# Optimization experiments

Hardware: AMD Instinct MI355X
Metric: run time of the kernel (lower is better)

Reference implementation:

```python
import jax, jax.numpy as jnp
import numpy as np

B, D, N, H = 4, 256, 2048, 4
HEAD_DIM = D // H


def conv1x1(W, b, x):
    # Conv1d(kernel_size=1): [B, Cin, N] -> [B, Cout, N]
    return jnp.einsum('oi,bin->bon', W, x) + b[None, :, None]


def setup_inputs() -> dict:
    key = jax.random.key(0)
    ks = jax.random.split(key, 8)
    s = 0.05
    return {
        'x': jax.random.normal(ks[0], (B, D, N), jnp.float32),
        'source': jax.random.normal(ks[1], (B, D, N), jnp.float32),
        'edge': jax.random.uniform(ks[2], (B, N, N), jnp.float32),
        'Wq': jax.random.normal(ks[3], (D, D), jnp.float32) * s,
        'bq': jnp.zeros((D,), jnp.float32),
        'Wk': jax.random.normal(ks[4], (D, D), jnp.float32) * s,
        'bk': jnp.zeros((D,), jnp.float32),
        'Wv': jax.random.normal(ks[5], (D, D), jnp.float32) * s,
        'bv': jnp.zeros((D,), jnp.float32),
        'Wm': jax.random.normal(ks[6], (D, D), jnp.float32) * s,
        'bm': jnp.zeros((D,), jnp.float32),
        'W1': jax.random.normal(ks[7], (2 * D, 2 * D), jnp.float32) * s,
        'b1': jnp.zeros((2 * D,), jnp.float32),
        'W2': jax.random.normal(jax.random.fold_in(key, 99), (D, 2 * D), jnp.float32) * s,
        'b2': jnp.zeros((D,), jnp.float32),
    }


def reference(x, source, edge, Wq, bq, Wk, bk, Wv, bv, Wm, bm, W1, b1, W2, b2):
    b = x.shape[0]
    # projections, then split channels D -> (head_dim, H), matching torch .view
    q = conv1x1(Wq, bq, x).reshape(b, HEAD_DIM, H, -1)       # [B, d, H, N]
    k = conv1x1(Wk, bk, source).reshape(b, HEAD_DIM, H, -1)  # [B, d, H, M]
    v = conv1x1(Wv, bv, source).reshape(b, HEAD_DIM, H, -1)
    scores = jnp.einsum('bdhn,bdhm->bhnm', q, k) / jnp.sqrt(jnp.float32(HEAD_DIM))
    prob = jax.nn.softmax(scores, axis=-1) * edge[:, None, :, :]  # edge-weighted probs
    msg = jnp.einsum('bhnm,bdhm->bdhn', prob, v).reshape(b, D, -1)
    message = conv1x1(Wm, bm, msg)                           # merge heads
    h = jnp.concatenate([x, message], axis=1)                # [B, 2D, N]
    h = jax.nn.relu(conv1x1(W1, b1, h))
    return conv1x1(W2, b2, h)                                # [B, D, N]
```

## Files before the change

kernel.cpp:

```cpp
#include <hip/hip_runtime.h>
#include <math.h>

#define B_ 4
#define D_ 256
#define N_ 2048
#define H_ 4

typedef __attribute__((ext_vector_type(8))) __bf16 bf16x8;
typedef __attribute__((ext_vector_type(4))) __bf16 bf16x4;
typedef __attribute__((ext_vector_type(4))) float f32x4;

__device__ __forceinline__ void load_row16(const float* src, bf16x8* xs) {
    float tmp[16];
    *(float4*)&tmp[0]  = *(const float4*)&src[0];
    *(float4*)&tmp[4]  = *(const float4*)&src[4];
    *(float4*)&tmp[8]  = *(const float4*)&src[8];
    *(float4*)&tmp[12] = *(const float4*)&src[12];
    __bf16* o = (__bf16*)xs;
#pragma unroll
    for (int i = 0; i < 16; ++i) o[i] = (__bf16)tmp[i];
}
__device__ __forceinline__ void load_row16(const __bf16* src, bf16x8* xs) {
    xs[0] = *(const bf16x8*)src;
    xs[1] = *(const bf16x8*)(src + 8);
}

template <typename In1T, typename In2T, typename OutT>
__device__ __forceinline__ void conv_tile(
    const In1T* __restrict__ in1, int C1,
    const In2T* __restrict__ in2, int C2,
    const float* __restrict__ Wt, const float* __restrict__ bias,
    OutT* __restrict__ out, int Cout, int K, int RELU, float oscale,
    int b, int o0, int n0, __bf16 (*sXT)[72])
{
    const int t = threadIdx.x;
    const int w  = t >> 6;
    const int g  = (t >> 4) & 3;
    const int c16 = t & 15;
    const int d_ld = t & 63;
    const int xcol = (t >> 6) * 16;

    f32x4 acc[4];
#pragma unroll
    for (int i = 0; i < 4; ++i) acc[i] = (f32x4){0.f, 0.f, 0.f, 0.f};

    bf16x8 xs[2];
    float4 wreg[4];
    const int ow = o0 + 16 * w + c16;

    auto LOADX = [&](int ks) {
        const int ch = ks + d_ld;
        if (ch < C1) load_row16(in1 + ((size_t)b * C1 + ch) * N_ + n0 + xcol, xs);
        else         load_row16(in2 + ((size_t)b * C2 + (ch - C1)) * N_ + n0 + xcol, xs);
    };
    auto LOADW = [&](int ks) {
        wreg[0] = *(const float4*)&Wt[(size_t)ow * K + ks + 8 * g];
        wreg[1] = *(const float4*)&Wt[(size_t)ow * K + ks + 8 * g + 4];
        wreg[2] = *(const float4*)&Wt[(size_t)ow * K + ks + 32 + 8 * g];
        wreg[3] = *(const float4*)&Wt[(size_t)ow * K + ks + 32 + 8 * g + 4];
    };
    auto WRITEXT = [&](int buf) {
        __bf16 (*sx)[72] = sXT + (size_t)buf * 64;
        const __bf16* kp = (const __bf16*)xs;
#pragma unroll
        for (int i = 0; i < 16; ++i)
            sx[xcol + i][d_ld] = kp[i];
    };

    LOADX(0);
    LOADW(0);
    WRITEXT(0);
    __syncthreads();

    const int nsteps = K >> 6;
    for (int s = 0; s < nsteps; ++s) {
        const int cur = s & 1;
        const int ks = s << 6;
        if (s + 1 < nsteps) LOADX(ks + 64);

        bf16x8 af[2];
#pragma unroll
        for (int kc = 0; kc < 2; ++kc) {
            const float* w0 = (const float*)&wreg[2 * kc];
            const float* w1 = (const float*)&wreg[2 * kc + 1];
#pragma unroll
            for (int i = 0; i < 4; ++i) {
                af[kc][i]     = (__bf16)w0[i];
                af[kc][i + 4] = (__bf16)w1[i];
            }
        }
        if (s + 1 < nsteps) LOADW(ks + 64);

        __bf16 (*sx)[72] = sXT + (size_t)cur * 64;
#pragma unroll
        for (int kc = 0; kc < 2; ++kc)
#pragma unroll
            for (int nsub = 0; nsub < 4; ++nsub) {
                const bf16x8 bfr = *(const bf16x8*)&sx[16 * nsub + c16][32 * kc + 8 * g];
                acc[nsub] = __builtin_amdgcn_mfma_f32_16x16x32_bf16(af[kc], bfr, acc[nsub], 0, 0, 0);
            }

        if (s + 1 < nsteps) WRITEXT(cur ^ 1);
        __syncthreads();
    }

#pragma unroll
    for (int nsub = 0; nsub < 4; ++nsub)
#pragma unroll
        for (int r = 0; r < 4; ++r) {
            const int o = o0 + 16 * w + 4 * g + r;
            float v = acc[nsub][r] + bias[o];
            if (RELU) v = fmaxf(v, 0.f);
            v *= oscale;
            out[((size_t)b * Cout + o) * N_ + n0 + 16 * nsub + c16] = (OutT)v;
        }
}

__global__ __launch_bounds__(256) void conv_hh_kernel(
    const __bf16* __restrict__ in1, const float* __restrict__ W,
    const float* __restrict__ bias, __bf16* __restrict__ out, int Cout, int K)
{
    __shared__ __bf16 sXT[2 * 64][72];
    conv_tile<__bf16, __bf16, __bf16>(in1, K, (const __bf16*)nullptr, 0,
        W, bias, out, Cout, K, 0, 1.0f,
        blockIdx.z, blockIdx.y * 64, blockIdx.x * 64, sXT);
}

__global__ __launch_bounds__(256) void conv_mix_kernel(
    const float* __restrict__ in1, int C1,
    const __bf16* __restrict__ in2, int C2,
    const float* __restrict__ W, const float* __restrict__ bias,
    __bf16* __restrict__ out, int Cout, int K)
{
    __shared__ __bf16 sXT[2 * 64][72];
    conv_tile<float, __bf16, __bf16>(in1, C1, in2, C2,
        W, bias, out, Cout, K, 1, 1.0f,
        blockIdx.z, blockIdx.y * 64, blockIdx.x * 64, sXT);
}

__global__ __launch_bounds__(256) void conv_hf_kernel(
    const __bf16* __restrict__ in1, const float* __restrict__ W,
    const float* __restrict__ bias, float* __restrict__ out, int Cout, int K)
{
    __shared__ __bf16 sXT[2 * 64][72];
    conv_tile<__bf16, __bf16, float>(in1, K, (const __bf16*)nullptr, 0,
        W, bias, out, Cout, K, 0, 1.0f,
        blockIdx.z, blockIdx.y * 64, blockIdx.x * 64, sXT);
}

__global__ __launch_bounds__(256) void qkv_conv_kernel(
    const float* __restrict__ x, const float* __restrict__ source,
    const float* __restrict__ Wq, const float* __restrict__ bq,
    const float* __restrict__ Wk, const float* __restrict__ bk,
    const float* __restrict__ Wv, const float* __restrict__ bv,
    __bf16* __restrict__ Qo, __bf16* __restrict__ Ko, __bf16* __restrict__ Vo)
{
    __shared__ __bf16 sXT[2 * 64][72];
    const int sel = blockIdx.y >> 2;
    const int o0  = (blockIdx.y & 3) * 64;
    const float* in = (sel == 0) ? x : source;
    const float* W  = (sel == 0) ? Wq : (sel == 1) ? Wk : Wv;
    const float* bs = (sel == 0) ? bq : (sel == 1) ? bk : bv;
    __bf16* out     = (sel == 0) ? Qo : (sel == 1) ? Ko : Vo;
    const float sc  = (sel == 1) ? 0.125f * 1.4426950408889634f : 1.0f;
    conv_tile<float, float, __bf16>(in, D_, (const float*)nullptr, 0,
        W, bs, out, D_, D_, 0, sc,
        blockIdx.z, o0, blockIdx.x * 64, sXT);
}

template <int NSPLIT>
__global__ __launch_bounds__(256, 4) void attn_kernel(
    const __bf16* __restrict__ Qg, const __bf16* __restrict__ Kg,
    const __bf16* __restrict__ Vg, const float* __restrict__ Eg,
    __bf16* __restrict__ OP, float* __restrict__ ML)
{
    const int nt    = blockIdx.x;
    const int n0    = nt * 64;
    const int split = blockIdx.y % NSPLIT;
    const int h     = blockIdx.y / NSPLIT;
    const int b     = blockIdx.z;
    const int t  = threadIdx.x;
    const int w  = t >> 6;
    const int g  = (t >> 4) & 3;
    const int c16 = t & 15;

    const int MT   = 32 / NSPLIT;
    const int m_lo = split * (N_ / NSPLIT);
    const int pid  = ((b * H_ + h) * NSPLIT + split) * 32 + nt;

    __shared__ __bf16 sKT[2][64][72];
    __shared__ __bf16 sP [2][64][72];

    bf16x8 qf[2];
#pragma unroll
    for (int kc = 0; kc < 2; ++kc)
#pragma unroll
        for (int e = 0; e < 8; ++e) {
            const int d = 32 * kc + 8 * g + e;
            qf[kc][e] = Qg[((size_t)b * D_ + d * H_ + h) * N_ + n0 + 16 * w + c16];
        }

    f32x4 acc[4];
#pragma unroll
    for (int i = 0; i < 4; ++i) acc[i] = (f32x4){0.f, 0.f, 0.f, 0.f};
    float Lr[4];
#pragma unroll
    for (int r = 0; r < 4; ++r) Lr[r] = 0.f;

    const int kd = t >> 2;
    const int km = (t & 3) * 16;
    const size_t kbase = ((size_t)b * D_ + kd * H_ + h) * N_ + m_lo + km;
    const size_t vrow  = ((size_t)b * D_ + (16 * w + c16) * H_ + h) * N_ + m_lo;
    const size_t ebase = ((size_t)b * N_ + n0 + 16 * w + 4 * g) * N_ + m_lo + c16;

    bf16x8 kreg[2];
    bf16x8 vreg[2];
    float  ereg[4][4];

    auto LOADK = [&](int m0) {
        kreg[0] = *(const bf16x8*)&Kg[kbase + m0];
        kreg[1] = *(const bf16x8*)&Kg[kbase + m0 + 8];
    };
    auto LOADV = [&](int m0) {
        vreg[0] = *(const bf16x8*)&Vg[vrow + m0 + 8 * g];
        vreg[1] = *(const bf16x8*)&Vg[vrow + m0 + 32 + 8 * g];
    };
    auto LOADE = [&](int m0) {
#pragma unroll
        for (int r = 0; r < 4; ++r)
#pragma unroll
            for (int ms = 0; ms < 4; ++ms)
                ereg[r][ms] = Eg[ebase + (size_t)r * N_ + m0 + 16 * ms];
    };
    const int kcb = kd >> 3, kcw = kd & 7;
    auto WRITEKT = [&](int buf) {
        const __bf16* kp = (const __bf16*)kreg;
#pragma unroll
        for (int i = 0; i < 16; ++i) {
            const int m = km + i;
            sKT[buf][m][(((kcb ^ ((m >> 3) & 7)) << 3) | kcw)] = kp[i];
        }
    };

    LOADK(0);
    LOADV(0);
    LOADE(0);
    WRITEKT(0);
    __syncthreads();

    for (int mt = 0; mt < MT; ++mt) {
        const int cur = mt & 1;
        const int m0n = (mt < MT - 1 ? mt + 1 : mt) * 64;

        const bf16x8 af0 = vreg[0], af1 = vreg[1];
        LOADK(m0n);
        LOADV(m0n);

        f32x4 sfrag[4];
#pragma unroll
        for (int msub = 0; msub < 4; ++msub) {
            const int m   = 16 * msub + c16;
            const int swz = (m >> 3) & 7;
            f32x4 s = (f32x4){0.f, 0.f, 0.f, 0.f};
#pragma unroll
            for (int kc = 0; kc < 2; ++kc) {
                const bf16x8 bfr = *(const bf16x8*)&sKT[cur][m][((4 * kc + g) ^ swz) << 3];
                s = __builtin_amdgcn_mfma_f32_16x16x32_bf16(qf[kc], bfr, s, 0, 0, 0);
            }
            sfrag[msub] = s;
        }

        {
            const int pc_hi = c16 >> 3, pc_lo = c16 & 7;
#pragma unroll
            for (int msub = 0; msub < 4; ++msub) {
#pragma unroll
                for (int r = 0; r < 4; ++r) {
                    const int nloc = 16 * w + 4 * g + r;
                    const int swz  = (nloc >> 3) & 7;
                    const float p = exp2f(sfrag[msub][r]);
                    Lr[r] += p;
                    sP[cur][nloc][((((2 * msub + pc_hi) ^ swz) << 3) | pc_lo)] =
                        (__bf16)(p * ereg[r][msub]);
                }
            }
        }
        LOADE(m0n);

        WRITEKT(cur ^ 1);
        __syncthreads();

#pragma unroll
        for (int nsub = 0; nsub < 4; ++nsub) {
            const int row = 16 * nsub + c16;
            const int swz = (row >> 3) & 7;
            const bf16x8 b0 = *(const bf16x8*)&sP[cur][row][(g ^ swz) << 3];
            acc[nsub] = __builtin_amdgcn_mfma_f32_16x16x32_bf16(af0, b0, acc[nsub], 0, 0, 0);
            const bf16x8 b1 = *(const bf16x8*)&sP[cur][row][((4 + g) ^ swz) << 3];
            acc[nsub] = __builtin_amdgcn_mfma_f32_16x16x32_bf16(af1, b1, acc[nsub], 0, 0, 0);
        }
    }

#pragma unroll
    for (int mask = 1; mask < 16; mask <<= 1)
#pragma unroll
        for (int r = 0; r < 4; ++r) Lr[r] += __shfl_xor(Lr[r], mask);
    if (c16 == 0) {
#pragma unroll
        for (int r = 0; r < 4; ++r) {
            const int nloc = 16 * w + 4 * g + r;
            ML[(size_t)pid * 128 + nloc]      = 0.0f;
            ML[(size_t)pid * 128 + 64 + nloc] = Lr[r];
        }
    }
#pragma unroll
    for (int nsub = 0; nsub < 4; ++nsub)
#pragma unroll
        for (int r = 0; r < 4; ++r) {
            const int dd = 16 * w + 4 * g + r;
            OP[(size_t)pid * 4096 + dd * 64 + 16 * nsub + c16] = (__bf16)acc[nsub][r];
        }
}

template <int NSPLIT>
__global__ __launch_bounds__(256) void combine_kernel(
    const __bf16* __restrict__ OP, const float* __restrict__ ML,
    __bf16* __restrict__ msg)
{
    const int nt = blockIdx.x;
    const int h  = blockIdx.y;
    const int b  = blockIdx.z;
    const int t  = threadIdx.x;
    const int d  = t & 63;
    const int seg = t >> 6;
    const int pid0 = ((b * H_ + h) * NSPLIT) * 32 + nt;

    __shared__ float sM[NSPLIT][64], sL[NSPLIT][64];
    if (t < NSPLIT * 64) {
        const int s = t >> 6, n = t & 63;
        sM[s][n] = ML[(size_t)(pid0 + s * 32) * 128 + n];
        sL[s][n] = ML[(size_t)(pid0 + s * 32) * 128 + 64 + n];
    }
    __syncthreads();

#pragma unroll
    for (int q = 0; q < 4; ++q) {
        const int c0 = seg * 16 + q * 4;
        float o[4] = {0.f, 0.f, 0.f, 0.f};
        float wgt[NSPLIT][4];
#pragma unroll
        for (int j = 0; j < 4; ++j) {
            float mx = -3.0e38f;
            for (int s = 0; s < NSPLIT; ++s) mx = fmaxf(mx, sM[s][c0 + j]);
            float den = 0.f;
            for (int s = 0; s < NSPLIT; ++s) {
                wgt[s][j] = __expf(sM[s][c0 + j] - mx);
                den += wgt[s][j] * sL[s][c0 + j];
            }
            const float inv = 1.0f / den;
            for (int s = 0; s < NSPLIT; ++s) wgt[s][j] *= inv;
        }
        for (int s = 0; s < NSPLIT; ++s) {
            const bf16x4 a = *(const bf16x4*)&OP[(size_t)(pid0 + s * 32) * 4096 + d * 64 + c0];
#pragma unroll
            for (int j = 0; j < 4; ++j) o[j] += wgt[s][j] * (float)a[j];
        }
        bf16x4 r;
#pragma unroll
        for (int j = 0; j < 4; ++j) r[j] = (__bf16)o[j];
        *(bf16x4*)&msg[((size_t)b * D_ + d * H_ + h) * N_ + nt * 64 + c0] = r;
    }
}

extern "C" void kernel_launch(void* const* d_in, const int* in_sizes, int n_in,
                              void* d_out, int out_size, void* d_ws, size_t ws_size,
                              hipStream_t stream) {
    const float* x      = (const float*)d_in[0];
    const float* source = (const float*)d_in[1];
    const float* edge   = (const float*)d_in[2];
    const float* Wq = (const float*)d_in[3];
    const float* bq = (const float*)d_in[4];
    const float* Wk = (const float*)d_in[5];
    const float* bk = (const float*)d_in[6];
    const float* Wv = (const float*)d_in[7];
    const float* bv = (const float*)d_in[8];
    const float* Wm = (const float*)d_in[9];
    const float* bm = (const float*)d_in[10];
    const float* W1 = (const float*)d_in[11];
    const float* b1 = (const float*)d_in[12];
    const float* W2 = (const float*)d_in[13];
    const float* b2 = (const float*)d_in[14];
    float* out = (float*)d_out;

    const size_t BDN = (size_t)B_ * D_ * N_;
    char* p = (char*)d_ws;
    __bf16* Qh  = (__bf16*)(p);
    __bf16* Kh  = (__bf16*)(p + 2 * BDN);
    __bf16* Vh  = (__bf16*)(p + 4 * BDN);
    __bf16* MSG = (__bf16*)(p + 6 * BDN);
    __bf16* MES = (__bf16*)(p + 8 * BDN);
    __bf16* H1  = (__bf16*)(p + 10 * BDN);
    char*   tail = p + 14 * BDN;
    const size_t baseBytes = 14 * BDN;

    const dim3 blk(256);
    const dim3 gD(N_ / 64, D_ / 64, B_);
    const dim3 g2D(N_ / 64, 2 * D_ / 64, B_);

    qkv_conv_kernel<<<dim3(N_ / 64, 12, B_), blk, 0, stream>>>(
        x, source, Wq, bq, Wk, bk, Wv, bv, Qh, Kh, Vh);

    auto needFor = [&](int ns) {
        const size_t pids = (size_t)ns * B_ * H_ * 32;
        return baseBytes + pids * 4096 * 2 + pids * 128 * 4;
    };
    if (ws_size >= needFor(2)) {
        const size_t pids = (size_t)2 * B_ * H_ * 32;
        __bf16* OP = (__bf16*)tail;
        float*  ML = (float*)(tail + pids * 4096 * 2);
        attn_kernel<2><<<dim3(32, H_ * 2, B_), blk, 0, stream>>>(Qh, Kh, Vh, edge, OP, ML);
        combine_kernel<2><<<dim3(32, H_, B_), blk, 0, stream>>>(OP, ML, MSG);
    } else {
        const size_t pids = (size_t)B_ * H_ * 32;
        __bf16* OP = (__bf16*)tail;
        float*  ML = (float*)(tail + pids * 4096 * 2);
        attn_kernel<1><<<dim3(32, H_, B_), blk, 0, stream>>>(Qh, Kh, Vh, edge, OP, ML);
        combine_kernel<1><<<dim3(32, H_, B_), blk, 0, stream>>>(OP, ML, MSG);
    }

    conv_hh_kernel<<<gD, blk, 0, stream>>>(MSG, Wm, bm, MES, D_, D_);
    conv_mix_kernel<<<g2D, blk, 0, stream>>>(x, D_, MES, D_, W1, b1, H1, 2 * D_, 2 * D_);
    conv_hf_kernel<<<gD, blk, 0, stream>>>(H1, W2, b2, out, D_, 2 * D_);
}
```

Baseline: 128.3 us.

## Fold merge-head conv weights into first MLP conv via precomputed W1·Wm

Precomputes a fused weight matrix Wcat = [W1_x | W1_m·Wm] and a fused bias b1 + W1_m·bm in a small per-call kernel. The merge-head conv kernel and its intermediate buffer are removed, and the MLP first layer reads the attention message directly. This removes one full conv pass and one bf16 round trip of the activation tensor, at the cost of a tiny weight GEMM each call and slightly different rounding, since the message is no longer rounded to bf16 after the merge.

```diff
diff --git a/kernel.cpp b/kernel.cpp
--- a/kernel.cpp
+++ b/kernel.cpp
@@ -114,16 +114,6 @@
             v *= oscale;
             out[((size_t)b * Cout + o) * N_ + n0 + 16 * nsub + c16] = (OutT)v;
         }
-}
-
-__global__ __launch_bounds__(256) void conv_hh_kernel(
-    const __bf16* __restrict__ in1, const float* __restrict__ W,
-    const float* __restrict__ bias, __bf16* __restrict__ out, int Cout, int K)
-{
-    __shared__ __bf16 sXT[2 * 64][72];
-    conv_tile<__bf16, __bf16, __bf16>(in1, K, (const __bf16*)nullptr, 0,
-        W, bias, out, Cout, K, 0, 1.0f,
-        blockIdx.z, blockIdx.y * 64, blockIdx.x * 64, sXT);
 }
 
 __global__ __launch_bounds__(256) void conv_mix_kernel(
@@ -166,6 +156,75 @@
     conv_tile<float, float, __bf16>(in, D_, (const float*)nullptr, 0,
         W, bs, out, D_, D_, 0, sc,
         blockIdx.z, o0, blockIdx.x * 64, sXT);
+}
+
+__global__ __launch_bounds__(256) void wfuse_kernel(
+    const float* __restrict__ W1, const float* __restrict__ Wm,
+    const float* __restrict__ bm, const float* __restrict__ b1,
+    float* __restrict__ Wcat, float* __restrict__ bfused)
+{
+    const int t = threadIdx.x;
+    if (blockIdx.y == 8) {
+        if (blockIdx.x < 2) {
+            const int o = blockIdx.x * 256 + t;
+            float a = b1[o];
+            for (int k = 0; k < 256; ++k)
+                a += W1[(size_t)o * 512 + 256 + k] * bm[k];
+            bfused[o] = a;
+        }
+        return;
+    }
+    const int o0 = blockIdx.y * 64;
+    const int c0 = blockIdx.x * 64;
+    const int tr = t >> 4, tc = t & 15;
+    if (c0 < 256) {
+#pragma unroll
+        for (int i = 0; i < 4; ++i) {
+            const int o = o0 + tr * 4 + i;
+            const float4 v = *(const float4*)&W1[(size_t)o * 512 + c0 + tc * 4];
+            *(float4*)&Wcat[(size_t)o * 512 + c0 + tc * 4] = v;
+        }
+        return;
+    }
+    __shared__ float sA[16][68];
+    __shared__ float sW[16][68];
+    float acc[4][4];
+#pragma unroll
+    for (int i = 0; i < 4; ++i)
+#pragma unroll
+        for (int j = 0; j < 4; ++j) acc[i][j] = 0.f;
+    const int wo = t & 63, wk = (t >> 6) * 4;
+    const int kr = t >> 4, cc = t & 15;
+    for (int k0 = 0; k0 < 256; k0 += 16) {
+        __syncthreads();
+        {
+            const float4 a = *(const float4*)&W1[(size_t)(o0 + wo) * 512 + 256 + k0 + wk];
+            sA[wk + 0][wo] = a.x; sA[wk + 1][wo] = a.y;
+            sA[wk + 2][wo] = a.z; sA[wk + 3][wo] = a.w;
+        }
+        {
+            const float4 wv = *(const float4*)&Wm[(size_t)(k0 + kr) * 256 + (c0 - 256) + cc * 4];
+            *(float4*)&sW[kr][cc * 4] = wv;
+        }
+        __syncthreads();
+#pragma unroll
+        for (int k = 0; k < 16; ++k) {
+            const float4 av = *(const float4*)&sA[k][tr * 4];
+            const float4 wv = *(const float4*)&sW[k][tc * 4];
+            const float aa[4] = {av.x, av.y, av.z, av.w};
+            const float ww[4] = {wv.x, wv.y, wv.z, wv.w};
+#pragma unroll
+            for (int i = 0; i < 4; ++i)
+#pragma unroll
+                for (int j = 0; j < 4; ++j)
+                    acc[i][j] = fmaf(aa[i], ww[j], acc[i][j]);
+        }
+    }
+#pragma unroll
+    for (int i = 0; i < 4; ++i) {
+        float4 r = {acc[i][0], acc[i][1], acc[i][2], acc[i][3]};
+        *(float4*)&Wcat[(size_t)(o0 + tr * 4 + i) * 512 + c0 + tc * 4] = r;
+    }
 }
 
 template <int NSPLIT>
@@ -398,37 +457,40 @@
     __bf16* Kh  = (__bf16*)(p + 2 * BDN);
     __bf16* Vh  = (__bf16*)(p + 4 * BDN);
     __bf16* MSG = (__bf16*)(p + 6 * BDN);
-    __bf16* MES = (__bf16*)(p + 8 * BDN);
-    __bf16* H1  = (__bf16*)(p + 10 * BDN);
-    char*   tail = p + 14 * BDN;
-    const size_t baseBytes = 14 * BDN;
+    __bf16* H1  = (__bf16*)(p + 8 * BDN);
+    char*   tail = p + 12 * BDN;
+    const size_t baseBytes = 12 * BDN;
 
     const dim3 blk(256);
     const dim3 gD(N_ / 64, D_ / 64, B_);
     const dim3 g2D(N_ / 64, 2 * D_ / 64, B_);
 
+    auto needFor = [&](int ns) {
+        const size_t pids = (size_t)ns * B_ * H_ * 32;
+        return baseBytes + pids * 4096 * 2 + pids * 128 * 4
+             + (size_t)512 * 512 * 4 + 512 * 4;
+    };
+
+    const int NS = (ws_size >= needFor(2)) ? 2 : 1;
+    const size_t pids = (size_t)NS * B_ * H_ * 32;
+    __bf16* OP = (__bf16*)tail;
+    float*  ML = (float*)(tail + pids * 4096 * 2);
+    float*  Wcat   = (float*)(tail + pids * 4096 * 2 + pids * 128 * 4);
+    float*  bfused = Wcat + (size_t)512 * 512;
+
+    wfuse_kernel<<<dim3(8, 9), blk, 0, stream>>>(W1, Wm, bm, b1, Wcat, bfused);
+
     qkv_conv_kernel<<<dim3(N_ / 64, 12, B_), blk, 0, stream>>>(
         x, source, Wq, bq, Wk, bk, Wv, bv, Qh, Kh, Vh);
 
-    auto needFor = [&](int ns) {
-        const size_t pids = (size_t)ns * B_ * H_ * 32;
-        return baseBytes + pids * 4096 * 2 + pids * 128 * 4;
-    };
-    if (ws_size >= needFor(2)) {
-        const size_t pids = (size_t)2 * B_ * H_ * 32;
-        __bf16* OP = (__bf16*)tail;
-        float*  ML = (float*)(tail + pids * 4096 * 2);
+    if (NS == 2) {
         attn_kernel<2><<<dim3(32, H_ * 2, B_), blk, 0, stream>>>(Qh, Kh, Vh, edge, OP, ML);
         combine_kernel<2><<<dim3(32, H_, B_), blk, 0, stream>>>(OP, ML, MSG);
     } else {
-        const size_t pids = (size_t)B_ * H_ * 32;
-        __bf16* OP = (__bf16*)tail;
-        float*  ML = (float*)(tail + pids * 4096 * 2);
         attn_kernel<1><<<dim3(32, H_, B_), blk, 0, stream>>>(Qh, Kh, Vh, edge, OP, ML);
         combine_kernel<1><<<dim3(32, H_, B_), blk, 0, stream>>>(OP, ML, MSG);
     }
 
-    conv_hh_kernel<<<gD, blk, 0, stream>>>(MSG, Wm, bm, MES, D_, D_);
-    conv_mix_kernel<<<g2D, blk, 0, stream>>>(x, D_, MES, D_, W1, b1, H1, 2 * D_, 2 * D_);
+    conv_mix_kernel<<<g2D, blk, 0, stream>>>(x, D_, MSG, D_, Wcat, bfused, H1, 2 * D_, 2 * D_);
     conv_hf_kernel<<<gD, blk, 0, stream>>>(H1, W2, b2, out, D_, 2 * D_);
 }
```

Result: slower. 137.0 us (+6.7%).

## Fuse split-combine of attention partials into message merge conv

Applied to the files above, without the earlier changes.

Removes the separate combine kernel and folds the combining of the attention split partials into the Wm 1x1 conv's input loader. The loader sums the partial outputs and divides by the summed L, which assumes the partial maxima are zero (attn writes M=0, since the softmax needs no max shift here). This drops one launch and the write/read round trip of the MSG buffer. In exchange, each conv block re-reads the partials and ML, and does that redundantly across the 4 output-channel tile blocks.

```diff
diff --git a/kernel.cpp b/kernel.cpp
--- a/kernel.cpp
+++ b/kernel.cpp
@@ -116,14 +116,132 @@
         }
 }
 
-__global__ __launch_bounds__(256) void conv_hh_kernel(
-    const __bf16* __restrict__ in1, const float* __restrict__ W,
-    const float* __restrict__ bias, __bf16* __restrict__ out, int Cout, int K)
+template <int NS>
+__global__ __launch_bounds__(256) void conv_msg_kernel(
+    const __bf16* __restrict__ OP, const float* __restrict__ ML,
+    const float* __restrict__ Wt, const float* __restrict__ bias,
+    __bf16* __restrict__ out)
 {
     __shared__ __bf16 sXT[2 * 64][72];
-    conv_tile<__bf16, __bf16, __bf16>(in1, K, (const __bf16*)nullptr, 0,
-        W, bias, out, Cout, K, 0, 1.0f,
-        blockIdx.z, blockIdx.y * 64, blockIdx.x * 64, sXT);
+    const int t = threadIdx.x;
+    const int w  = t >> 6;
+    const int g  = (t >> 4) & 3;
+    const int c16 = t & 15;
+    const int d_ld = t & 63;
+    const int xcol = (t >> 6) * 16;
+    const int nt = blockIdx.x;
+    const int n0 = nt * 64;
+    const int o0 = blockIdx.y * 64;
+    const int b  = blockIdx.z;
+    const int K = D_, Cout = D_;
+
+    const int h = d_ld & 3;
+    const size_t pid0 = ((size_t)(b * H_ + h) * NS) * 32 + nt;
+
+    float invL[16];
+#pragma unroll
+    for (int i = 0; i < 16; i += 4) {
+        float4 a = *(const float4*)&ML[pid0 * 128 + 64 + xcol + i];
+        if (NS == 2) {
+            const float4 c = *(const float4*)&ML[(pid0 + 32) * 128 + 64 + xcol + i];
+            a.x += c.x; a.y += c.y; a.z += c.z; a.w += c.w;
+        }
+        invL[i + 0] = 1.0f / a.x; invL[i + 1] = 1.0f / a.y;
+        invL[i + 2] = 1.0f / a.z; invL[i + 3] = 1.0f / a.w;
+    }
+
+    f32x4 acc[4];
+#pragma unroll
+    for (int i = 0; i < 4; ++i) acc[i] = (f32x4){0.f, 0.f, 0.f, 0.f};
+
+    bf16x8 xs[2];
+    float4 wreg[4];
+    const int ow = o0 + 16 * w + c16;
+
+    auto LOADX = [&](int ks) {
+        const int dd = (ks + d_ld) >> 2;
+        const __bf16* p0 = &OP[pid0 * 4096 + dd * 64 + xcol];
+        const bf16x8 a0 = *(const bf16x8*)p0;
+        const bf16x8 a1 = *(const bf16x8*)(p0 + 8);
+        bf16x8 b0, b1;
+        if (NS == 2) {
+            const __bf16* p1 = &OP[(pid0 + 32) * 4096 + dd * 64 + xcol];
+            b0 = *(const bf16x8*)p1;
+            b1 = *(const bf16x8*)(p1 + 8);
+        }
+        __bf16* o = (__bf16*)xs;
+#pragma unroll
+        for (int i = 0; i < 8; ++i) {
+            float v = (float)a0[i];
+            if (NS == 2) v += (float)b0[i];
+            o[i] = (__bf16)(v * invL[i]);
+        }
+#pragma unroll
+        for (int i = 0; i < 8; ++i) {
+            float v = (float)a1[i];
+            if (NS == 2) v += (float)b1[i];
+            o[8 + i] = (__bf16)(v * invL[8 + i]);
+        }
+    };
+    auto LOADW = [&](int ks) {
+        wreg[0] = *(const float4*)&Wt[(size_t)ow * K + ks + 8 * g];
+        wreg[1] = *(const float4*)&Wt[(size_t)ow * K + ks + 8 * g + 4];
+        wreg[2] = *(const float4*)&Wt[(size_t)ow * K + ks + 32 + 8 * g];
+        wreg[3] = *(const float4*)&Wt[(size_t)ow * K + ks + 32 + 8 * g + 4];
+    };
+    auto WRITEXT = [&](int buf) {
+        __bf16 (*sx)[72] = sXT + (size_t)buf * 64;
+        const __bf16* kp = (const __bf16*)xs;
+#pragma unroll
+        for (int i = 0; i < 16; ++i)
+            sx[xcol + i][d_ld] = kp[i];
+    };
+
+    LOADX(0);
+    LOADW(0);
+    WRITEXT(0);
+    __syncthreads();
+
+    const int nsteps = K >> 6;
+    for (int s = 0; s < nsteps; ++s) {
+        const int cur = s & 1;
+        const int ks = s << 6;
+        if (s + 1 < nsteps) LOADX(ks + 64);
+
+        bf16x8 af[2];
+#pragma unroll
+        for (int kc = 0; kc < 2; ++kc) {
+            const float* w0 = (const float*)&wreg[2 * kc];
+            const float* w1 = (const float*)&wreg[2 * kc + 1];
+#pragma unroll
+            for (int i = 0; i < 4; ++i) {
+                af[kc][i]     = (__bf16)w0[i];
+                af[kc][i + 4] = (__bf16)w1[i];
+            }
+        }
+        if (s + 1 < nsteps) LOADW(ks + 64);
+
+        __bf16 (*sx)[72] = sXT + (size_t)cur * 64;
+#pragma unroll
+        for (int kc = 0; kc < 2; ++kc)
+#pragma unroll
+            for (int nsub = 0; nsub < 4; ++nsub) {
+                const bf16x8 bfr = *(const bf16x8*)&sx[16 * nsub + c16][32 * kc + 8 * g];
+                acc[nsub] = __builtin_amdgcn_mfma_f32_16x16x32_bf16(af[kc], bfr, acc[nsub], 0, 0, 0);
+            }
+
+        if (s + 1 < nsteps) WRITEXT(cur ^ 1);
+        __syncthreads();
+    }
+
+#pragma unroll
+    for (int nsub = 0; nsub < 4; ++nsub)
+#pragma unroll
+        for (int r = 0; r < 4; ++r) {
+            const int o = o0 + 16 * w + 4 * g + r;
+            const float v = acc[nsub][r] + bias[o];
+            out[((size_t)b * Cout + o) * N_ + n0 + 16 * nsub + c16] = (__bf16)v;
+        }
 }
 
 __global__ __launch_bounds__(256) void conv_mix_kernel(
@@ -320,56 +438,6 @@
             const int dd = 16 * w + 4 * g + r;
             OP[(size_t)pid * 4096 + dd * 64 + 16 * nsub + c16] = (__bf16)acc[nsub][r];
         }
-}
-
-template <int NSPLIT>
-__global__ __launch_bounds__(256) void combine_kernel(
-    const __bf16* __restrict__ OP, const float* __restrict__ ML,
-    __bf16* __restrict__ msg)
-{
-    const int nt = blockIdx.x;
-    const int h  = blockIdx.y;
-    const int b  = blockIdx.z;
-    const int t  = threadIdx.x;
-    const int d  = t & 63;
-    const int seg = t >> 6;
-    const int pid0 = ((b * H_ + h) * NSPLIT) * 32 + nt;
-
-    __shared__ float sM[NSPLIT][64], sL[NSPLIT][64];
-    if (t < NSPLIT * 64) {
-        const int s = t >> 6, n = t & 63;
-        sM[s][n] = ML[(size_t)(pid0 + s * 32) * 128 + n];
-        sL[s][n] = ML[(size_t)(pid0 + s * 32) * 128 + 64 + n];
-    }
-    __syncthreads();
-
-#pragma unroll
-    for (int q = 0; q < 4; ++q) {
-        const int c0 = seg * 16 + q * 4;
-        float o[4] = {0.f, 0.f, 0.f, 0.f};
-        float wgt[NSPLIT][4];
-#pragma unroll
-        for (int j = 0; j < 4; ++j) {
-            float mx = -3.0e38f;
-            for (int s = 0; s < NSPLIT; ++s) mx = fmaxf(mx, sM[s][c0 + j]);
-            float den = 0.f;
-            for (int s = 0; s < NSPLIT; ++s) {
-                wgt[s][j] = __expf(sM[s][c0 + j] - mx);
-                den += wgt[s][j] * sL[s][c0 + j];
-            }
-            const float inv = 1.0f / den;
-            for (int s = 0; s < NSPLIT; ++s) wgt[s][j] *= inv;
-        }
-        for (int s = 0; s < NSPLIT; ++s) {
-            const bf16x4 a = *(const bf16x4*)&OP[(size_t)(pid0 + s * 32) * 4096 + d * 64 + c0];
-#pragma unroll
-            for (int j = 0; j < 4; ++j) o[j] += wgt[s][j] * (float)a[j];
-        }
-        bf16x4 r;
-#pragma unroll
-        for (int j = 0; j < 4; ++j) r[j] = (__bf16)o[j];
-        *(bf16x4*)&msg[((size_t)b * D_ + d * H_ + h) * N_ + nt * 64 + c0] = r;
-    }
 }
 
 extern "C" void kernel_launch(void* const* d_in, const int* in_sizes, int n_in,
@@ -397,38 +465,36 @@
     __bf16* Qh  = (__bf16*)(p);
     __bf16* Kh  = (__bf16*)(p + 2 * BDN);
     __bf16* Vh  = (__bf16*)(p + 4 * BDN);
-    __bf16* MSG = (__bf16*)(p + 6 * BDN);
-    __bf16* MES = (__bf16*)(p + 8 * BDN);
-    __bf16* H1  = (__bf16*)(p + 10 * BDN);
-    char*   tail = p + 14 * BDN;
-    const size_t baseBytes = 14 * BDN;
+    __bf16* MES = (__bf16*)(p + 6 * BDN);
+    __bf16* H1  = (__bf16*)(p + 8 * BDN);
+    char*   tail = p + 12 * BDN;
+    const size_t baseBytes = 12 * BDN;
 
     const dim3 blk(256);
     const dim3 gD(N_ / 64, D_ / 64, B_);
     const dim3 g2D(N_ / 64, 2 * D_ / 64, B_);
 
-    qkv_conv_kernel<<<dim3(N_ / 64, 12, B_), blk, 0, stream>>>(
-        x, source, Wq, bq, Wk, bk, Wv, bv, Qh, Kh, Vh);
-
     auto needFor = [&](int ns) {
         const size_t pids = (size_t)ns * B_ * H_ * 32;
         return baseBytes + pids * 4096 * 2 + pids * 128 * 4;
     };
-    if (ws_size >= needFor(2)) {
-        const size_t pids = (size_t)2 * B_ * H_ * 32;
-        __bf16* OP = (__bf16*)tail;
-        float*  ML = (float*)(tail + pids * 4096 * 2);
+
+    const int NS = (ws_size >= needFor(2)) ? 2 : 1;
+    const size_t pids = (size_t)NS * B_ * H_ * 32;
+    __bf16* OP = (__bf16*)tail;
+    float*  ML = (float*)(tail + pids * 4096 * 2);
+
+    qkv_conv_kernel<<<dim3(N_ / 64, 12, B_), blk, 0, stream>>>(
+        x, source, Wq, bq, Wk, bk, Wv, bv, Qh, Kh, Vh);
+
+    if (NS == 2) {
         attn_kernel<2><<<dim3(32, H_ * 2, B_), blk, 0, stream>>>(Qh, Kh, Vh, edge, OP, ML);
-        combine_kernel<2><<<dim3(32, H_, B_), blk, 0, stream>>>(OP, ML, MSG);
+        conv_msg_kernel<2><<<gD, blk, 0, stream>>>(OP, ML, Wm, bm, MES);
     } else {
-        const size_t pids = (size_t)B_ * H_ * 32;
-        __bf16* OP = (__bf16*)tail;
-        float*  ML = (float*)(tail + pids * 4096 * 2);
         attn_kernel<1><<<dim3(32, H_, B_), blk, 0, stream>>>(Qh, Kh, Vh, edge, OP, ML);
-        combine_kernel<1><<<dim3(32, H_, B_), blk, 0, stream>>>(OP, ML, MSG);
+        conv_msg_kernel<1><<<gD, blk, 0, stream>>>(OP, ML, Wm, bm, MES);
     }
 
-    conv_hh_kernel<<<gD, blk, 0, stream>>>(MSG, Wm, bm, MES, D_, D_);
     conv_mix_kernel<<<g2D, blk, 0, stream>>>(x, D_, MES, D_, W1, b1, H1, 2 * D_, 2 * D_);
     conv_hf_kernel<<<gD, blk, 0, stream>>>(H1, W2, b2, out, D_, 2 * D_);
 }
```

Result: no change. 126.6 us, median of 2 (-1.4%).
